# Performance work log

Hardware: AMD Instinct MI355X
Metric: run time of the kernel (lower is better)

The kernel has to match this reference:

```python
import jax, jax.numpy as jnp
import numpy as np

V, B, T, R, U, L, S = 8000, 64, 256, 1024, 512, 3, 1024


def setup_inputs() -> dict:
    key = jax.random.key(0)
    ks = jax.random.split(key, 12)
    sd = 0.05
    stdv = float(np.sqrt(1.0 / V))
    return {
        "input_data": jax.random.randint(ks[0], (B, T), 0, V, dtype=jnp.int32),
        "targets": jax.random.randint(ks[1], (B, T), 0, V, dtype=jnp.int32),
        "sampled": jax.random.randint(ks[2], (S,), 0, V, dtype=jnp.int32),
        "true_expected_counts": jax.random.uniform(ks[3], (B * T,), minval=0.01, maxval=1.0),
        "sampled_expected_counts": jax.random.uniform(ks[4], (S,), minval=0.01, maxval=1.0),
        "embedding": jax.random.uniform(ks[5], (V, U), minval=-stdv, maxval=stdv),
        "Wh0": jax.random.normal(ks[6], (U + R, R)) * sd,
        "bh0": jnp.zeros((R,)),
        "Wt0": jax.random.normal(ks[7], (U + R, R)) * sd,
        "bt0": -jnp.ones((R,)),  # bias_start = -1.0 for transform gate
        "Wh": jax.random.normal(ks[8], (L - 1, R, R)) * sd,
        "bh": jnp.zeros((L - 1, R)),
        "Wt": jax.random.normal(ks[9], (L - 1, R, R)) * sd,
        "bt": -jnp.ones((L - 1, R)),
        "Wp": jax.random.normal(ks[10], (R, U)) * sd,
        "bp": jnp.zeros((U,)),
        "softmax_w": jax.random.normal(ks[11], (V, U)) * sd,
        "softmax_b": jnp.zeros((V,)),
    }


def reference(input_data, targets, sampled, true_expected_counts,
              sampled_expected_counts, embedding, Wh0, bh0, Wt0, bt0,
              Wh, bh, Wt, bt, Wp, bp, softmax_w, softmax_b):
    # embedding lookup (keep_prob=1.0 -> input dropout is a no-op)
    x = embedding[input_data]              # [B,T,U]
    xs = jnp.transpose(x, (1, 0, 2))       # [T,B,U] for time-major scan

    def step(state, xt):
        # highway layer 0: sees [input, state]
        cat = jnp.concatenate([xt, state], axis=1)       # [B,U+R]
        h = jnp.tanh(cat @ Wh0 + bh0)
        t = jax.nn.sigmoid(cat @ Wt0 + bt0)
        state = (h - state) * t + state
        # highway layers 1..L-1: state only
        for l in range(L - 1):
            h = jnp.tanh(state @ Wh[l] + bh[l])
            t = jax.nn.sigmoid(state @ Wt[l] + bt[l])
            state = (h - state) * t + state
        return state, state

    state0 = jnp.zeros((B, R), dtype=x.dtype)
    final_state, states = jax.lax.scan(step, state0, xs)   # states: [T,B,R]

    # OutputProjectionWrapper: per-step linear rnn_size -> num_units
    outputs = states @ Wp + bp                              # [T,B,U]
    outputs = jnp.transpose(outputs, (1, 0, 2)).reshape(B * T, U)

    # sampled softmax loss (fixed candidates, remove accidental hits)
    labels = targets.reshape(-1)                            # [N]
    w_true = softmax_w[labels]                              # [N,U]
    b_true = softmax_b[labels]                              # [N]
    true_logits = jnp.sum(outputs * w_true, axis=-1) + b_true \
        - jnp.log(true_expected_counts)                     # [N]
    sampled_logits = outputs @ softmax_w[sampled].T + softmax_b[sampled] \
        - jnp.log(sampled_expected_counts)                  # [N,S]
    acc_hit = labels[:, None] == sampled[None, :]
    sampled_logits = jnp.where(acc_hit, sampled_logits - 1e9, sampled_logits)

    logits = jnp.concatenate([true_logits[:, None], sampled_logits], axis=1)
    loss = -jax.nn.log_softmax(logits, axis=1)[:, 0]        # true class at idx 0
    cost = jnp.mean(loss)
    return cost
```

## Files before the change

### kernel.cpp

```cpp
#include <hip/hip_runtime.h>
#include <hip/hip_bf16.h>
#include <hip/hip_fp16.h>

#define Vv 8000
#define Bb 64
#define Tt 256
#define Rr 1024
#define Uu 512
#define Ll 3
#define Sn 1024
#define Nrows (Bb*Tt)
#define NCG 32
#define NCH 8
#define NWG2 (NCG*NCH)
#define NSLOT 6
#define CNTSTRIDE 1024

typedef __attribute__((ext_vector_type(8))) short short8;
typedef __attribute__((ext_vector_type(4))) float f32x4;
typedef __attribute__((ext_vector_type(4))) unsigned int u32x4;
typedef unsigned long long u64t;

static __device__ inline f32x4 mfma16(short8 a, short8 b, f32x4 c) {
    return __builtin_amdgcn_mfma_f32_16x16x32_bf16(a, b, c, 0, 0, 0);
}

static __device__ inline float bf2f(unsigned short u) {
    union { unsigned int i; float f; } v; v.i = ((unsigned int)u) << 16; return v.f;
}
static __device__ inline unsigned short f2bf(float f) {
    union { float f; unsigned int i; } v; v.f = f;
    unsigned int x = v.i;
    unsigned int r = (x + 0x7fffu + ((x >> 16) & 1u)) >> 16;
    return (unsigned short)r;
}
static __device__ inline unsigned short f2h(float f) {
    __half h = __float2half(f);
    union { __half h; unsigned short u; } v; v.h = h; return v.u;
}
static __device__ inline float h2f(unsigned short u) {
    union { unsigned short u; __half h; } v; v.u = u; return __half2float(v.h);
}

#if __has_builtin(__builtin_amdgcn_rcpf)
#define RCPF(x) __builtin_amdgcn_rcpf(x)
#else
#define RCPF(x) (1.0f/(x))
#endif

static __device__ __forceinline__ void ldg16_coh(u32x4* d, u64t a) {
    asm volatile("global_load_dwordx4 %0, %1, off sc0 sc1" : "=v"(*d) : "v"(a));
}
static __device__ __forceinline__ void wait_vm0_8(u32x4& a, u32x4& b, u32x4& c, u32x4& d,
                                                  u32x4& e, u32x4& f, u32x4& g, u32x4& h) {
    asm volatile("s_waitcnt vmcnt(0)"
                 : "+v"(a), "+v"(b), "+v"(c), "+v"(d),
                   "+v"(e), "+v"(f), "+v"(g), "+v"(h) :: "memory");
}
static __device__ __forceinline__ void atom_pk_f16(u64t a, unsigned v) {
    asm volatile("global_atomic_pk_add_f16 %0, %1, off" :: "v"(a), "v"(v) : "memory");
}
static __device__ __forceinline__ void st4_zero_coh(u64t a) {
    asm volatile("global_store_dword %0, %1, off sc0 sc1" :: "v"(a), "v"(0u) : "memory");
}
static __device__ __forceinline__ unsigned ld_flag_coh(const unsigned int* p) {
    unsigned v;
    asm volatile("global_load_dword %0, %1, off sc0 sc1\n\ts_waitcnt vmcnt(0)"
                 : "=v"(v) : "v"((u64t)p) : "memory");
    return v;
}

__global__ __launch_bounds__(256) void detect_kernel(const unsigned short* __restrict__ tec,
                                                     int* __restrict__ flag) {
    __shared__ int cnt;
    if (threadIdx.x == 0) cnt = 0;
    __syncthreads();
    float f = bf2f(tec[threadIdx.x]);
    int ok = (f >= 0.0078125f && f <= 1.0f) ? 1 : 0;
    atomicAdd(&cnt, ok);
    __syncthreads();
    if (threadIdx.x == 0) *flag = (cnt >= 240) ? 0 : 1;
}

__global__ __launch_bounds__(256) void cvt_kernel(const void* __restrict__ src,
                                                  unsigned short* __restrict__ dst,
                                                  int n, const int* __restrict__ flag) {
    int i = blockIdx.x * 256 + threadIdx.x;
    if (i >= n) return;
    if (*flag)
        dst[i] = f2bf(((const float*)src)[i]);
    else
        dst[i] = ((const unsigned short*)src)[i];
}

__global__ __launch_bounds__(256) void pack_direct(const unsigned short* __restrict__ W,
                                                   short* __restrict__ dst,
                                                   int KT, int NT, int N) {
    int tid = blockIdx.x * 256 + threadIdx.x;
    int total = KT * NT * 64;
    if (tid >= total) return;
    int lane = tid & 63;
    int tile = tid >> 6;
    int nt = tile % NT;
    int kt = tile / NT;
    int k0 = kt * 32 + (lane >> 4) * 8;
    int n  = nt * 16 + (lane & 15);
    short8 v;
#pragma unroll
    for (int j = 0; j < 8; ++j)
        v[j] = (short)W[(size_t)(k0 + j) * N + n];
    ((short8*)dst)[tid] = v;
}

__global__ __launch_bounds__(256) void pack_gather(const void* __restrict__ sw,
                                                   const int* __restrict__ sampled,
                                                   short* __restrict__ dst,
                                                   const int* __restrict__ flag) {
    int tid = blockIdx.x * 256 + threadIdx.x;
    int total = 16 * 64 * 64;
    if (tid >= total) return;
    int lane = tid & 63;
    int tile = tid >> 6;
    int nt = tile % 64;
    int kt = tile / 64;
    int k0 = kt * 32 + (lane >> 4) * 8;
    int n  = nt * 16 + (lane & 15);
    int row = sampled[n];
    short8 v;
    if (*flag) {
        const float* swf = (const float*)sw;
#pragma unroll
        for (int j = 0; j < 8; ++j)
            v[j] = (short)f2bf(swf[(size_t)row * Uu + k0 + j]);
    } else {
        const unsigned short* swu = (const unsigned short*)sw;
#pragma unroll
        for (int j = 0; j < 8; ++j)
            v[j] = (short)swu[(size_t)row * Uu + k0 + j];
    }
    ((short8*)dst)[tid] = v;
}

static __device__ __forceinline__ void slice_arrive(unsigned int* cnt) {
    __syncthreads();
    if (threadIdx.x == 0)
        __hip_atomic_fetch_add(cnt, 1u, __ATOMIC_RELAXED, __HIP_MEMORY_SCOPE_AGENT);
}
static __device__ __forceinline__ void slice_wait(unsigned int* cnt, unsigned int tgt) {
    if (threadIdx.x == 0) {
        if (ld_flag_coh(cnt) < tgt) {
            do {
                __builtin_amdgcn_s_sleep(8);
            } while (ld_flag_coh(cnt) < tgt);
        }
    }
    __syncthreads();
}

__global__ __launch_bounds__(256, 1) void scan_kernel(
    const short8* __restrict__ pWh0, const short8* __restrict__ pWt0,
    const short8* __restrict__ pWh1, const short8* __restrict__ pWt1,
    const short8* __restrict__ pWh2, const short8* __restrict__ pWt2,
    const unsigned short* __restrict__ cbh0, const unsigned short* __restrict__ cbt0,
    const unsigned short* __restrict__ cbh,  const unsigned short* __restrict__ cbt,
    const unsigned short* __restrict__ embb, const int* __restrict__ tokens,
    unsigned int* __restrict__ acc, unsigned short* __restrict__ hist,
    unsigned int* cnt)
{
    __shared__ short8 Wlds[14 * 4 * 64];

    int tid  = threadIdx.x;
    int lane = tid & 63, wave = tid >> 6;
    int quad = lane >> 4, l15 = lane & 15;
    int ch = blockIdx.x & 7;
    int cg = blockIdx.x >> 3;
    int rowA = wave * 16 + l15;

    {
        int nt  = cg * 2 + (wave & 1);
        int isT = wave >> 1;
#pragma unroll
        for (int i = 0; i < 14; ++i) {
            const short8* src;
            int kt_g;
            if (i < 2)       { src = isT ? pWt0 : pWh0; kt_g = 2 * ch + i; }
            else if (i < 6)  { src = isT ? pWt0 : pWh0; kt_g = 16 + 4 * ch + (i - 2); }
            else if (i < 10) { src = isT ? pWt1 : pWh1; kt_g = 4 * ch + (i - 6); }
            else             { src = isT ? pWt2 : pWh2; kt_g = 4 * ch + (i - 10); }
            Wlds[i * 256 + tid] = src[((size_t)kt_g * 64 + nt) * 64 + lane];
        }
    }
    __syncthreads();

    short8 bh8v[3][4], bt8v[3][4];
#pragma unroll
    for (int s = 0; s < 4; ++s) {
        int col0 = ch * 128 + s * 32 + quad * 8;
        bh8v[0][s] = *(const short8*)(cbh0 + col0);
        bt8v[0][s] = *(const short8*)(cbt0 + col0);
        bh8v[1][s] = *(const short8*)(cbh + col0);
        bt8v[1][s] = *(const short8*)(cbt + col0);
        bh8v[2][s] = *(const short8*)(cbh + 1024 + col0);
        bt8v[2][s] = *(const short8*)(cbt + 1024 + col0);
    }
    int zbase = blockIdx.x * 256 + tid;

    float sreg[4][8];
    short8 a1r[4], a2r[4];
#pragma unroll
    for (int s = 0; s < 4; ++s) {
#pragma unroll
        for (int jj = 0; jj < 8; ++jj) { sreg[s][jj] = 0.f; a1r[s][jj] = 0; a2r[s][jj] = 0; }
    }

    f32x4 eH[2] = {{0,0,0,0},{0,0,0,0}};
    f32x4 eT[2] = {{0,0,0,0},{0,0,0,0}};
    {
        int token0 = tokens[rowA * Tt];
#pragma unroll
        for (int s = 0; s < 2; ++s) {
            short8 ae = *(const short8*)(embb + (size_t)token0 * Uu
                                         + ch * 64 + s * 32 + quad * 8);
#pragma unroll
            for (int c = 0; c < 2; ++c) {
                eH[c] = mfma16(ae, Wlds[s * 256 + c * 64 + lane], eH[c]);
                eT[c] = mfma16(ae, Wlds[s * 256 + (2 + c) * 64 + lane], eT[c]);
            }
        }
    }

    unsigned int ph = 0;
    int slot = 0;
    for (int t = 0; t < Tt; ++t) {
#pragma unroll
        for (int l = 0; l < 3; ++l) {
            f32x4 aH[2], aT[2];
            int slot0 = (l == 0) ? 2 : (l == 1 ? 6 : 10);
            if (l == 0) {
#pragma unroll
                for (int c = 0; c < 2; ++c) { aH[c] = eH[c]; aT[c] = eT[c]; }
            } else {
#pragma unroll
                for (int c = 0; c < 2; ++c) {
                    aH[c] = (f32x4){0,0,0,0}; aT[c] = (f32x4){0,0,0,0};
                }
            }
#pragma unroll
            for (int s = 0; s < 4; ++s) {
#pragma unroll
                for (int c = 0; c < 2; ++c) {
                    short8 bH = Wlds[(slot0 + s) * 256 + c * 64 + lane];
                    short8 bT = Wlds[(slot0 + s) * 256 + (2 + c) * 64 + lane];
                    aH[c] = mfma16(a1r[s], bH, aH[c]);
                    aH[c] = mfma16(a2r[s], bH, aH[c]);
                    aT[c] = mfma16(a1r[s], bT, aT[c]);
                    aT[c] = mfma16(a2r[s], bT, aT[c]);
                }
            }

            unsigned int* accS = acc + (size_t)slot * 65536;
#pragma unroll
            for (int c = 0; c < 2; ++c) {
                int col = cg * 32 + c * 16 + l15;
#pragma unroll
                for (int r = 0; r < 4; ++r) {
                    int row = wave * 16 + quad * 4 + r;
                    unsigned d = ((unsigned)f2h(aT[c][r]) << 16) | (unsigned)f2h(aH[c][r]);
                    atom_pk_f16((u64t)(accS + row * 1024 + col), d);
                }
            }

            ++ph;
            slice_arrive(cnt + (cg >> 2) * CNTSTRIDE);
            if (l == 2) {
                int tn = (t + 1 < Tt) ? t + 1 : t;
                int token = tokens[rowA * Tt + tn];
#pragma unroll
                for (int c = 0; c < 2; ++c) {
                    eH[c] = (f32x4){0,0,0,0}; eT[c] = (f32x4){0,0,0,0};
                }
#pragma unroll
                for (int s = 0; s < 2; ++s) {
                    short8 ae = *(const short8*)(embb + (size_t)token * Uu
                                                 + ch * 64 + s * 32 + quad * 8);
#pragma unroll
                    for (int c = 0; c < 2; ++c) {
                        eH[c] = mfma16(ae, Wlds[s * 256 + c * 64 + lane], eH[c]);
                        eT[c] = mfma16(ae, Wlds[s * 256 + (2 + c) * 64 + lane], eT[c]);
                    }
                }
            }
            {
                int zsl = (slot >= 3) ? slot - 3 : slot + 3;
                st4_zero_coh((u64t)(acc + (size_t)zsl * 65536 + zbase));
            }
            slice_wait(cnt + ch * CNTSTRIDE, 32u * ph);

            u32x4 rr[4][2];
#pragma unroll
            for (int s = 0; s < 4; ++s) {
                int col0 = ch * 128 + s * 32 + quad * 8;
                const unsigned int* p = accS + rowA * 1024 + col0;
                ldg16_coh(&rr[s][0], (u64t)p);
                ldg16_coh(&rr[s][1], (u64t)(p + 4));
            }
            wait_vm0_8(rr[0][0], rr[0][1], rr[1][0], rr[1][1],
                       rr[2][0], rr[2][1], rr[3][0], rr[3][1]);
#pragma unroll
            for (int s = 0; s < 4; ++s) {
                int col0 = ch * 128 + s * 32 + quad * 8;
                short8 bh8 = bh8v[l][s];
                short8 bt8 = bt8v[l][s];
                unsigned dv[8];
                *(u32x4*)&dv[0] = rr[s][0]; *(u32x4*)&dv[4] = rr[s][1];
                short8 hbv;
#pragma unroll
                for (int jj = 0; jj < 8; ++jj) {
                    float hv = h2f((unsigned short)(dv[jj] & 0xffffu));
                    float tv = h2f((unsigned short)(dv[jj] >> 16));
                    float sO = sreg[s][jj];
                    float xh = hv + bf2f((unsigned short)bh8[jj]);
                    float eh = __expf(xh + xh);
                    float hh = 1.0f - 2.0f * RCPF(eh + 1.0f);
                    float xt = tv + bf2f((unsigned short)bt8[jj]);
                    float gg = RCPF(1.0f + __expf(-xt));
                    float sn = (hh - sO) * gg + sO;
                    sreg[s][jj] = sn;
                    unsigned short hb = f2bf(sn);
                    a1r[s][jj] = (short)hb;
                    a2r[s][jj] = (short)f2bf(sn - bf2f(hb));
                    hbv[jj] = (short)hb;
                }
                if (l == 2 && cg == 0)
                    *(short8*)(hist + (size_t)t * (Bb * Rr) + rowA * Rr + col0) = hbv;
            }
            slot = (slot == 5) ? 0 : slot + 1;
        }
    }
}

__global__ __launch_bounds__(256) void proj_kernel(
    const unsigned short* __restrict__ hist, const short8* __restrict__ pB,
    const unsigned short* __restrict__ bp, unsigned short* __restrict__ proj)
{
    int lane = threadIdx.x & 63, wave = threadIdx.x >> 6;
    int quad = lane >> 4, l15 = lane & 15;
    int m0 = blockIdx.x * 64 + wave * 16;
    int n0 = blockIdx.y * 64;
    f32x4 acc[4];
#pragma unroll
    for (int c = 0; c < 4; ++c) acc[c] = (f32x4){0.f, 0.f, 0.f, 0.f};

    const unsigned short* arow = hist + (size_t)(m0 + l15) * Rr;
    for (int kt = 0; kt < 32; ++kt) {
        short8 a = *(const short8*)(arow + kt * 32 + quad * 8);
#pragma unroll
        for (int c = 0; c < 4; ++c) {
            short8 b = pB[((size_t)kt * 32 + (n0 >> 4) + c) * 64 + lane];
            acc[c] = mfma16(a, b, acc[c]);
        }
    }
#pragma unroll
    for (int c = 0; c < 4; ++c) {
        int col = n0 + c * 16 + l15;
        float bpv = bf2f(bp[col]);
#pragma unroll
        for (int r = 0; r < 4; ++r) {
            int row = m0 + quad * 4 + r;
            proj[(size_t)row * Uu + col] = f2bf(acc[c][r] + bpv);
        }
    }
}

__global__ __launch_bounds__(256) void sampled_kernel(
    const unsigned short* __restrict__ proj, const short8* __restrict__ pB,
    const unsigned short* __restrict__ sb, const int* __restrict__ sampled,
    const int* __restrict__ targets, const unsigned short* __restrict__ sec,
    unsigned short* __restrict__ slog)
{
    int lane = threadIdx.x & 63, wave = threadIdx.x >> 6;
    int quad = lane >> 4, l15 = lane & 15;
    int m0 = blockIdx.x * 64 + wave * 16;
    int n0 = blockIdx.y * 64;
    f32x4 acc[4];
#pragma unroll
    for (int c = 0; c < 4; ++c) acc[c] = (f32x4){0.f, 0.f, 0.f, 0.f};

    const unsigned short* arow = proj + (size_t)(m0 + l15) * Uu;
    for (int kt = 0; kt < 16; ++kt) {
        short8 a = *(const short8*)(arow + kt * 32 + quad * 8);
#pragma unroll
        for (int c = 0; c < 4; ++c) {
            short8 b = pB[((size_t)kt * 64 + (n0 >> 4) + c) * 64 + lane];
            acc[c] = mfma16(a, b, acc[c]);
        }
    }
#pragma unroll
    for (int c = 0; c < 4; ++c) {
        int j = n0 + c * 16 + l15;
        int sj = sampled[j];
        float bias = bf2f(sb[sj]) - logf(bf2f(sec[j]));
#pragma unroll
        for (int r = 0; r < 4; ++r) {
            int row = m0 + quad * 4 + r;
            int n_idx = ((row & 63) << 8) + (row >> 6);
            int label = targets[n_idx];
            float lg = acc[c][r] + bias;
            if (label == sj) lg = -30000.0f;
            slog[(size_t)row * Sn + j] = f2h(lg);
        }
    }
}

__global__ __launch_bounds__(256) void true_kernel(
    const unsigned short* __restrict__ proj, const void* __restrict__ sw,
    const unsigned short* __restrict__ sb, const int* __restrict__ targets,
    const unsigned short* __restrict__ tec, float* __restrict__ tl,
    const int* __restrict__ flagp)
{
    int lane = threadIdx.x & 63;
    int m = blockIdx.x * 4 + (threadIdx.x >> 6);
    int n_idx = ((m & 63) << 8) + (m >> 6);
    int label = targets[n_idx];
    short8 a = *(const short8*)(proj + (size_t)m * Uu + lane * 8);
    float s = 0.f;
    if (*flagp) {
        const float* bw = (const float*)sw + (size_t)label * Uu + lane * 8;
        float4 b0 = *(const float4*)bw;
        float4 b1 = *(const float4*)(bw + 4);
        float bb[8] = {b0.x, b0.y, b0.z, b0.w, b1.x, b1.y, b1.z, b1.w};
#pragma unroll
        for (int j = 0; j < 8; ++j)
            s += bf2f((unsigned short)a[j]) * bb[j];
    } else {
        short8 b = *(const short8*)((const unsigned short*)sw + (size_t)label * Uu + lane * 8);
#pragma unroll
        for (int j = 0; j < 8; ++j)
            s += bf2f((unsigned short)a[j]) * bf2f((unsigned short)b[j]);
    }
#pragma unroll
    for (int mask = 32; mask >= 1; mask >>= 1) s += __shfl_xor(s, mask);
    if (lane == 0)
        tl[m] = s + bf2f(sb[label]) - logf(bf2f(tec[n_idx]));
}

__global__ __launch_bounds__(256) void lse_kernel(
    const unsigned short* __restrict__ slog, const float* __restrict__ tl,
    float* __restrict__ loss_sum)
{
    int lane = threadIdx.x & 63;
    int m = blockIdx.x * 4 + (threadIdx.x >> 6);
    const short8* p = (const short8*)(slog + (size_t)m * Sn);
    short8 v0 = p[lane * 2];
    short8 v1 = p[lane * 2 + 1];
    float v[16];
#pragma unroll
    for (int j = 0; j < 8; ++j) { v[j] = h2f((unsigned short)v0[j]); v[8 + j] = h2f((unsigned short)v1[j]); }
    float mx = v[0];
#pragma unroll
    for (int j = 1; j < 16; ++j) mx = fmaxf(mx, v[j]);
#pragma unroll
    for (int mask = 32; mask >= 1; mask >>= 1) mx = fmaxf(mx, __shfl_xor(mx, mask));
    float se = 0.f;
#pragma unroll
    for (int j = 0; j < 16; ++j) se += expf(v[j] - mx);
#pragma unroll
    for (int mask = 32; mask >= 1; mask >>= 1) se += __shfl_xor(se, mask);
    if (lane == 0) {
        float tlv = tl[m];
        float mm  = fmaxf(mx, tlv);
        float tot = se * expf(mx - mm) + expf(tlv - mm);
        atomicAdd(loss_sum, mm + logf(tot) - tlv);
    }
}

__global__ void fin_kernel(const float* __restrict__ loss_sum, unsigned int* __restrict__ out) {
    float v = loss_sum[0] * (1.0f / (float)Nrows);
    unsigned int H = (unsigned int)f2bf(v);
    out[0] = (H << 16) | H;
}

extern "C" void kernel_launch(void* const* d_in, const int* in_sizes, int n_in,
                              void* d_out, int out_size, void* d_ws, size_t ws_size,
                              hipStream_t stream) {
    (void)in_sizes; (void)n_in; (void)out_size; (void)ws_size;

    const int*  input_data = (const int*)d_in[0];
    const int*  targets    = (const int*)d_in[1];
    const int*  sampled    = (const int*)d_in[2];
    const void* tec        = d_in[3];
    const void* sec        = d_in[4];
    const void* emb        = d_in[5];
    const void* Wh0        = d_in[6];
    const void* bh0        = d_in[7];
    const void* Wt0        = d_in[8];
    const void* bt0        = d_in[9];
    const void* Wh         = d_in[10];
    const void* bh         = d_in[11];
    const void* Wt         = d_in[12];
    const void* bt         = d_in[13];
    const void* Wp         = d_in[14];
    const void* bp         = d_in[15];
    const void* sw         = d_in[16];
    const void* sb         = d_in[17];

    char* ws = (char*)d_ws;
    size_t off = 0;
    short* pWh0 = (short*)(ws + off); off += (size_t)48 * 64 * 512 * 2;
    short* pWt0 = (short*)(ws + off); off += (size_t)48 * 64 * 512 * 2;
    short* pWh1 = (short*)(ws + off); off += (size_t)32 * 64 * 512 * 2;
    short* pWh2 = (short*)(ws + off); off += (size_t)32 * 64 * 512 * 2;
    short* pWt1 = (short*)(ws + off); off += (size_t)32 * 64 * 512 * 2;
    short* pWt2 = (short*)(ws + off); off += (size_t)32 * 64 * 512 * 2;
    short* pWp  = (short*)(ws + off); off += (size_t)32 * 32 * 512 * 2;
    short* pSW  = (short*)(ws + off); off += (size_t)16 * 64 * 512 * 2;
    unsigned short* cbh0 = (unsigned short*)(ws + off); off += 1024 * 2;
    unsigned short* cbt0 = (unsigned short*)(ws + off); off += 1024 * 2;
    unsigned short* cbh  = (unsigned short*)(ws + off); off += 2048 * 2;
    unsigned short* cbt  = (unsigned short*)(ws + off); off += 2048 * 2;
    unsigned short* cbp  = (unsigned short*)(ws + off); off += 512 * 2;
    unsigned short* csb  = (unsigned short*)(ws + off); off += 8000 * 2;
    unsigned short* ctec = (unsigned short*)(ws + off); off += 16384 * 2;
    unsigned short* csec = (unsigned short*)(ws + off); off += 1024 * 2;
    unsigned int* acc = (unsigned int*)(ws + off); off += (size_t)NSLOT * 65536 * 4;
    unsigned short* hist = (unsigned short*)(ws + off); off += (size_t)Nrows * Rr * 2;
    unsigned short* proj = (unsigned short*)(ws + off); off += (size_t)Nrows * Uu * 2;
    unsigned short* slog = (unsigned short*)(ws + off); off += (size_t)Nrows * Sn * 2;
    float* tl   = (float*)(ws + off); off += (size_t)Nrows * 4;
    float* loss = (float*)(ws + off); off += 256;
    int*   flag = (int*)(ws + off);   off += 256;
    off = (off + 4095) & ~(size_t)4095;
    unsigned int* barrier_mem = (unsigned int*)(ws + off); off += 8 * 4096;

    unsigned int* cnt = barrier_mem;

    unsigned short* cWh0 = (unsigned short*)slog;
    unsigned short* cWt0 = cWh0 + (size_t)1536 * 1024;
    unsigned short* cWh  = cWt0 + (size_t)1536 * 1024;
    unsigned short* cWt  = cWh  + (size_t)2 * 1024 * 1024;
    unsigned short* cWp  = cWt  + (size_t)2 * 1024 * 1024;
    unsigned short* embb = (unsigned short*)proj;

    hipMemsetAsync(acc, 0, (size_t)NSLOT * 65536 * 4, stream);
    hipMemsetAsync(loss, 0, 4, stream);
    hipMemsetAsync(barrier_mem, 0, 8 * 4096, stream);

    detect_kernel<<<1, 256, 0, stream>>>((const unsigned short*)tec, flag);
#define CVT(src, dst, n) cvt_kernel<<<((n) + 255) / 256, 256, 0, stream>>>(src, dst, n, flag)
    CVT(bh0, cbh0, 1024);
    CVT(bt0, cbt0, 1024);
    CVT(bh,  cbh,  2048);
    CVT(bt,  cbt,  2048);
    CVT(bp,  cbp,  512);
    CVT(sb,  csb,  8000);
    CVT(tec, ctec, 16384);
    CVT(sec, csec, 1024);
    CVT(emb, embb, 8000 * 512);
    CVT(Wh0, cWh0, 1536 * 1024);
    CVT(Wt0, cWt0, 1536 * 1024);
    CVT(Wh,  cWh,  2 * 1024 * 1024);
    CVT(Wt,  cWt,  2 * 1024 * 1024);
    CVT(Wp,  cWp,  1024 * 512);
#undef CVT

    pack_direct<<<(48 * 64 * 64 + 255) / 256, 256, 0, stream>>>(cWh0, pWh0, 48, 64, 1024);
    pack_direct<<<(48 * 64 * 64 + 255) / 256, 256, 0, stream>>>(cWt0, pWt0, 48, 64, 1024);
    pack_direct<<<(32 * 64 * 64 + 255) / 256, 256, 0, stream>>>(cWh,               pWh1, 32, 64, 1024);
    pack_direct<<<(32 * 64 * 64 + 255) / 256, 256, 0, stream>>>(cWh + 1024 * 1024, pWh2, 32, 64, 1024);
    pack_direct<<<(32 * 64 * 64 + 255) / 256, 256, 0, stream>>>(cWt,               pWt1, 32, 64, 1024);
    pack_direct<<<(32 * 64 * 64 + 255) / 256, 256, 0, stream>>>(cWt + 1024 * 1024, pWt2, 32, 64, 1024);
    pack_direct<<<(32 * 32 * 64 + 255) / 256, 256, 0, stream>>>(cWp, pWp, 32, 32, 512);
    pack_gather<<<(16 * 64 * 64 + 255) / 256, 256, 0, stream>>>(sw, sampled, pSW, flag);

    scan_kernel<<<NWG2, 256, 0, stream>>>(
        (const short8*)pWh0, (const short8*)pWt0,
        (const short8*)pWh1, (const short8*)pWt1,
        (const short8*)pWh2, (const short8*)pWt2,
        cbh0, cbt0, cbh, cbt,
        embb, input_data,
        acc, hist, cnt);

    proj_kernel<<<dim3(256, 8), 256, 0, stream>>>(hist, (const short8*)pWp, cbp, proj);
    true_kernel<<<Nrows / 4, 256, 0, stream>>>(proj, sw, csb, targets, ctec, tl, flag);
    sampled_kernel<<<dim3(256, 16), 256, 0, stream>>>(proj, (const short8*)pSW, csb,
                                                      sampled, targets, csec, slog);
    lse_kernel<<<Nrows / 4, 256, 0, stream>>>(slog, tl, loss);
    fin_kernel<<<1, 1, 0, stream>>>(loss, (unsigned int*)d_out);
}
```

Baseline: 4.301 ms.

## Replace block-level slice barriers with per-wave counters in scan kernel

Swaps the block-wide __syncthreads plus single-thread atomic arrive/wait for per-wave arrival counters. Each wave now signals and polls only the counter for its own row band, and the zeroing of stale accumulator slots is remapped so each wave clears only its own rows. The aim is to remove intra-block serialization in the recurrent step and let waves proceed independently. In exchange it uses four times as many counters, more atomic traffic, and a shorter sleep while spinning. Correctness depends on per-wave row ownership matching exactly.

Result: slower. 4.477 ms (+4.1%).

```diff
diff --git a/kernel.cpp b/kernel.cpp
--- a/kernel.cpp
+++ b/kernel.cpp
@@ -141,20 +141,15 @@
     ((short8*)dst)[tid] = v;
 }
 
-static __device__ __forceinline__ void slice_arrive(unsigned int* cnt) {
-    __syncthreads();
-    if (threadIdx.x == 0)
-        __hip_atomic_fetch_add(cnt, 1u, __ATOMIC_RELAXED, __HIP_MEMORY_SCOPE_AGENT);
-}
-static __device__ __forceinline__ void slice_wait(unsigned int* cnt, unsigned int tgt) {
-    if (threadIdx.x == 0) {
-        if (ld_flag_coh(cnt) < tgt) {
-            do {
-                __builtin_amdgcn_s_sleep(8);
-            } while (ld_flag_coh(cnt) < tgt);
-        }
-    }
-    __syncthreads();
+static __device__ __forceinline__ void wave_arrive(unsigned int* c) {
+    asm volatile("s_waitcnt vmcnt(0)" ::: "memory");
+    if ((threadIdx.x & 63) == 0)
+        __hip_atomic_fetch_add(c, 1u, __ATOMIC_RELAXED, __HIP_MEMORY_SCOPE_AGENT);
+}
+static __device__ __forceinline__ void wave_wait(unsigned int* c, unsigned int tgt) {
+    if (ld_flag_coh(c) < tgt) {
+        do { __builtin_amdgcn_s_sleep(2); } while (ld_flag_coh(c) < tgt);
+    }
 }
 
 __global__ __launch_bounds__(256, 1) void scan_kernel(
@@ -203,7 +198,12 @@
         bh8v[2][s] = *(const short8*)(cbh + 1024 + col0);
         bt8v[2][s] = *(const short8*)(cbt + 1024 + col0);
     }
-    int zbase = blockIdx.x * 256 + tid;
+
+    int zidx = blockIdx.x * 64 + lane;
+    int zoff = (wave * 16 + (zidx >> 10)) * 1024 + (zidx & 1023);
+
+    unsigned int* arr_cnt  = cnt + ((cg >> 2) * 4 + wave) * CNTSTRIDE;
+    unsigned int* wait_cnt = cnt + (ch * 4 + wave) * CNTSTRIDE;
 
     float sreg[4][8];
     short8 a1r[4], a2r[4];
@@ -271,7 +271,7 @@
             }
 
             ++ph;
-            slice_arrive(cnt + (cg >> 2) * CNTSTRIDE);
+            wave_arrive(arr_cnt);
             if (l == 2) {
                 int tn = (t + 1 < Tt) ? t + 1 : t;
                 int token = tokens[rowA * Tt + tn];
@@ -292,9 +292,9 @@
             }
             {
                 int zsl = (slot >= 3) ? slot - 3 : slot + 3;
-                st4_zero_coh((u64t)(acc + (size_t)zsl * 65536 + zbase));
-            }
-            slice_wait(cnt + ch * CNTSTRIDE, 32u * ph);
+                st4_zero_coh((u64t)(acc + (size_t)zsl * 65536 + zoff));
+            }
+            wave_wait(wait_cnt, 32u * ph);
 
             u32x4 rr[4][2];
 #pragma unroll
@@ -530,7 +530,7 @@
     float* loss = (float*)(ws + off); off += 256;
     int*   flag = (int*)(ws + off);   off += 256;
     off = (off + 4095) & ~(size_t)4095;
-    unsigned int* barrier_mem = (unsigned int*)(ws + off); off += 8 * 4096;
+    unsigned int* barrier_mem = (unsigned int*)(ws + off); off += 32 * 4096;
 
     unsigned int* cnt = barrier_mem;
 
@@ -543,7 +543,7 @@
 
     hipMemsetAsync(acc, 0, (size_t)NSLOT * 65536 * 4, stream);
     hipMemsetAsync(loss, 0, 4, stream);
-    hipMemsetAsync(barrier_mem, 0, 8 * 4096, stream);
+    hipMemsetAsync(barrier_mem, 0, 32 * 4096, stream);
 
     detect_kernel<<<1, 256, 0, stream>>>((const unsigned short*)tec, flag);
 #define CVT(src, dst, n) cvt_kernel<<<((n) + 255) / 256, 256, 0, stream>>>(src, dst, n, flag)
```
